# Kernel tuning notes

Measured on AMD Instinct MI355X. Metric: run time of the kernel, lower is better.

The kernel has to match this reference:

```python
import jax, jax.numpy as jnp
import numpy as np

B, S, D = 4, 2048, 1024

def setup_inputs() -> dict:
    key = jax.random.key(0)
    k1, k2, k3, k4 = jax.random.split(key, 4)
    x = jax.random.normal(k1, (B, S, D), dtype=jnp.float32)
    # module init: jr.normal(key, (dim, dim)) / 40
    Qw = jax.random.normal(k2, (D, D), dtype=jnp.float32) / 40
    Kw = jax.random.normal(k3, (D, D), dtype=jnp.float32) / 40
    Vw = jax.random.normal(k4, (D, D), dtype=jnp.float32) / 40
    return {"x": x, "Qw": Qw, "Kw": Kw, "Vw": Vw}

def reference(x, Qw, Kw, Vw):
    # Q/K/V projections: [B,S,D] @ [D,D] -> [B,S,D]
    Q = x @ Qw
    K = x @ Kw
    V = x @ Vw
    d = x.shape[-1]
    S_len = x.shape[-2]
    # causal additive mask: 0 on/below diagonal, -inf above
    mask = jnp.where(jnp.tril(jnp.ones((S_len, S_len), dtype=x.dtype)) == 0,
                     -jnp.inf, 0.0).astype(x.dtype)
    # scores: [B,S,S]
    scores = jnp.einsum('bqd,bkd->bqk', Q, K) / jnp.sqrt(jnp.asarray(d, x.dtype))
    scores = scores + mask
    attn = jax.nn.softmax(scores, axis=-1)
    return jnp.einsum('bqk,bkd->bqd', attn, V)
```

## Files before the change

kernel.cpp:

```cpp
#include <hip/hip_runtime.h>
#include <hip/hip_bf16.h>

typedef __attribute__((ext_vector_type(8))) __bf16 bf16x8;
typedef __attribute__((ext_vector_type(4))) float f32x4;

#define BM 128
#define BN 128
#define BK 64

__device__ inline unsigned short f2bf(float f) {
    union { float f; unsigned u; } v; v.f = f;
    unsigned r = (v.u + 0x7FFFu + ((v.u >> 16) & 1u)) >> 16;
    return (unsigned short)r;
}

__device__ __forceinline__ void gld16(const void* g, void* l) {
    __builtin_amdgcn_global_load_lds(
        (const __attribute__((address_space(1))) unsigned int*)g,
        (__attribute__((address_space(3))) unsigned int*)l, 16, 0, 0);
}

__global__ void detect_dtype(const unsigned short* __restrict__ x, int* __restrict__ flag)
{
    const int tid = threadIdx.x;
    int cnt = 0;
    for (int i = tid; i < 1024; i += 256) {
        unsigned e = (x[2 * i] >> 7) & 0xFFu;
        cnt += (e >= 0x60u && e <= 0x88u) ? 1 : 0;
    }
    #pragma unroll
    for (int o = 32; o >= 1; o >>= 1) cnt += __shfl_xor(cnt, o, 64);
    __shared__ int red[4];
    if ((tid & 63) == 0) red[tid >> 6] = cnt;
    __syncthreads();
    if (tid == 0) {
        int t = red[0] + red[1] + red[2] + red[3];
        *flag = (t >= 512) ? 0 : 1;
    }
}

__global__ __launch_bounds__(256, 2)
void gemm_bt(const unsigned short* __restrict__ A, const unsigned short* __restrict__ Bt,
             void* __restrict__ Call, int K, int lda, int ldb, int ldc,
             long oA, long oB, long oC, long sA, long sB, long sC,
             float scale, int mode, int q0,
             const int* __restrict__ dtf, int outKind)
{
    const int dt = *dtf;
    const int z = blockIdx.z;
    const long aBase = oA + (long)z * sA;
    const long bBase = oB + (long)z * sB;
    const long cBase = oC + (long)z * sC;

    int mt, nt;
    {
        const int nwg = gridDim.x * gridDim.y;
        int lin = blockIdx.y * gridDim.x + blockIdx.x;
        const int q = nwg >> 3, r = nwg & 7;
        const int xcd = lin & 7, idx = lin >> 3;
        lin = (xcd < r ? xcd * (q + 1) : r * (q + 1) + (xcd - r) * q) + idx;
        if (mode == 1) {
            int rem = lin, rr = 0, w = q0 / BN + 1;
            while (rem >= w) { rem -= w; rr++; w++; }
            mt = rr; nt = rem;
        } else { mt = lin / gridDim.x; nt = lin % gridDim.x; }
    }
    const int m0 = mt * BM;
    const int n0 = nt * BN;
    int kmax = K;
    if (mode == 2) kmax = min(K, q0 + m0 + BM);

    __shared__ __align__(16) short As[2][BM * BK];
    __shared__ __align__(16) short Bs[2][BN * BK];

    const int tid  = threadIdx.x;
    const int wave = tid >> 6;
    const int lane = tid & 63;
    const int wm = (wave >> 1) * 64;
    const int wn = (wave & 1) * 64;
    const int lrow = lane & 15;
    const int quad = lane >> 4;

    const int sRow = lane >> 3;
    const int sCol = ((lane & 7) ^ sRow) * 8;
    const long gA = aBase + (long)(m0 + wave * 32 + sRow) * lda + sCol;
    const long gB = bBase + (long)(n0 + wave * 32 + sRow) * ldb + sCol;

    auto stage = [&](int buf, int k0) {
        short* dA = &As[buf][wave * 32 * BK];
        short* dB = &Bs[buf][wave * 32 * BK];
        const unsigned short* pA = A + gA + k0;
        const unsigned short* pB = Bt + gB + k0;
        #pragma unroll
        for (int c = 0; c < 4; c++) {
            gld16(pA + (long)(c * 8) * lda, dA + c * 8 * BK);
            gld16(pB + (long)(c * 8) * ldb, dB + c * 8 * BK);
        }
    };

    f32x4 acc[4][4];
    #pragma unroll
    for (int i = 0; i < 4; i++)
        #pragma unroll
        for (int j = 0; j < 4; j++) {
            f32x4 zero = {0.f, 0.f, 0.f, 0.f};
            acc[i][j] = zero;
        }

    const int rq  = lrow & 7;
    const int pc0 = (quad ^ rq) * 8;
    const int pc1 = ((quad + 4) ^ rq) * 8;

    stage(0, 0);
    __syncthreads();
    int cur = 0;

    for (int k0 = 0; k0 < kmax; k0 += BK) {
        const int kn = k0 + BK;
        if (kn < kmax) stage(cur ^ 1, kn);

        const short* rA = &As[cur][0];
        const short* rB = &Bs[cur][0];
        bf16x8 af[4], bfr[4];
        #pragma unroll
        for (int i = 0; i < 4; i++) {
            af[i]  = *(const bf16x8*)&rA[(wm + i * 16 + lrow) * BK + pc0];
            bfr[i] = *(const bf16x8*)&rB[(wn + i * 16 + lrow) * BK + pc0];
        }
        #pragma unroll
        for (int i = 0; i < 4; i++)
            #pragma unroll
            for (int j = 0; j < 4; j++)
                acc[i][j] = __builtin_amdgcn_mfma_f32_16x16x32_bf16(af[i], bfr[j], acc[i][j], 0, 0, 0);
        #pragma unroll
        for (int i = 0; i < 4; i++) {
            af[i]  = *(const bf16x8*)&rA[(wm + i * 16 + lrow) * BK + pc1];
            bfr[i] = *(const bf16x8*)&rB[(wn + i * 16 + lrow) * BK + pc1];
        }
        #pragma unroll
        for (int i = 0; i < 4; i++)
            #pragma unroll
            for (int j = 0; j < 4; j++)
                acc[i][j] = __builtin_amdgcn_mfma_f32_16x16x32_bf16(af[i], bfr[j], acc[i][j], 0, 0, 0);

        __syncthreads();
        cur ^= 1;
    }

    const int oF32 = (outKind == 1) | ((outKind == 2) & dt);
    #pragma unroll
    for (int i = 0; i < 4; i++) {
        const int mr = m0 + wm + i * 16 + quad * 4;
        #pragma unroll
        for (int j = 0; j < 4; j++) {
            const int nc = n0 + wn + j * 16 + lrow;
            #pragma unroll
            for (int r = 0; r < 4; r++) {
                const long ofs = cBase + (long)(mr + r) * ldc + nc;
                const float v = acc[i][j][r] * scale;
                if (oF32) ((float*)Call)[ofs] = v;
                else      ((unsigned short*)Call)[ofs] = f2bf(v);
            }
        }
    }
}

__global__ __launch_bounds__(256)
void xpose_cast(const void* __restrict__ src, unsigned short* __restrict__ dT,
                unsigned short* __restrict__ dC, int R, int C,
                long oS, long sS, long sDT, long sDC,
                const int* __restrict__ dtf, int srcExt)
{
    const int dt = srcExt ? *dtf : 0;
    const int b = blockIdx.z;
    const long sb = oS + (long)b * sS;
    __shared__ unsigned short t[64][65];
    const int c0 = blockIdx.x * 64, r0 = blockIdx.y * 64;
    const int tid = threadIdx.x;
    #pragma unroll
    for (int it = 0; it < 16; it++) {
        int idx = it * 256 + tid;
        int r = idx >> 6, c = idx & 63;
        long e = sb + (long)(r0 + r) * C + (c0 + c);
        unsigned short v = dt ? f2bf(((const float*)src)[e]) : ((const unsigned short*)src)[e];
        t[r][c] = v;
        if (dC) dC[(long)b * sDC + (long)(r0 + r) * C + (c0 + c)] = v;
    }
    if (!dT) return;
    __syncthreads();
    #pragma unroll
    for (int it = 0; it < 16; it++) {
        int idx = it * 256 + tid;
        int r = idx >> 6, c = idx & 63;
        dT[(long)b * sDT + (long)(c0 + r) * R + (r0 + c)] = t[c][r];
    }
}

__global__ __launch_bounds__(256)
void softmax_causal(float* __restrict__ Sc, int S, int CH, int q0)
{
    const int r = blockIdx.x, z = blockIdx.y;
    float* srow = Sc + ((long)z * CH + r) * S;
    unsigned short* prow = (unsigned short*)srow;
    const int n = q0 + r + 1;
    const int limit = q0 + (r & ~(BM - 1)) + BM;
    const int tid = threadIdx.x;
    const int lane = tid & 63, wave = tid >> 6;
    __shared__ float red[4];

    float v[8];
    float lm = -1e30f;
    #pragma unroll
    for (int c = 0; c < 8; c++) {
        int j = c * 256 + tid;
        v[c] = (j < n) ? srow[j] : -1e30f;
        lm = fmaxf(lm, v[c]);
    }
    #pragma unroll
    for (int o = 32; o >= 1; o >>= 1) lm = fmaxf(lm, __shfl_xor(lm, o, 64));
    if (lane == 0) red[wave] = lm;
    __syncthreads();
    const float m = fmaxf(fmaxf(red[0], red[1]), fmaxf(red[2], red[3]));
    __syncthreads();

    float ev[8];
    float ls = 0.f;
    #pragma unroll
    for (int c = 0; c < 8; c++) {
        int j = c * 256 + tid;
        float e = (j < n) ? __expf(v[c] - m) : 0.f;
        ev[c] = e;
        ls += e;
    }
    #pragma unroll
    for (int o = 32; o >= 1; o >>= 1) ls += __shfl_xor(ls, o, 64);
    if (lane == 0) red[wave] = ls;
    __syncthreads();
    const float inv = 1.0f / (red[0] + red[1] + red[2] + red[3]);

    #pragma unroll
    for (int c = 0; c < 8; c++) {
        int j = c * 256 + tid;
        if (j < limit) prow[j] = f2bf(j < n ? ev[c] * inv : 0.f);
    }
}

__global__ __launch_bounds__(256)
void fill_zero(void* o, long n, const int* dtf)
{
    long i = (long)blockIdx.x * 256 + threadIdx.x;
    if (i < n) {
        if (*dtf) ((float*)o)[i] = 0.f;
        else ((unsigned short*)o)[i] = 0;
    }
}

extern "C" void kernel_launch(void* const* d_in, const int* in_sizes, int n_in,
                              void* d_out, int out_size, void* d_ws, size_t ws_size,
                              hipStream_t stream)
{
    const int B = 4, S = 2048, D = 1024;
    const void* x  = d_in[0];
    const void* Qw = d_in[1];
    const void* Kw = d_in[2];
    const void* Vw = d_in[3];
    (void)in_sizes; (void)n_in; (void)out_size;

    int* dtf = (int*)d_ws;
    char* p = (char*)d_ws + 4096;
    const size_t MB = (size_t)1 << 20;

    detect_dtype<<<1, 256, 0, stream>>>((const unsigned short*)x, dtf);

    const long nOut = (long)B * S * D;

    const size_t needA = 4096 + 36 * MB + (size_t)B * S * S * 4;
    if (ws_size >= needA) {
        unsigned short* QwB = (unsigned short*)p;
        unsigned short* KwB = (unsigned short*)(p + 2 * MB);
        unsigned short* Xb  = (unsigned short*)(p + 4 * MB);
        unsigned short* Buf = (unsigned short*)(p + 20 * MB);
        float* Sc = (float*)(p + 36 * MB);
        unsigned short* WT  = (unsigned short*)Sc;
        unsigned short* VwT = QwB;
        unsigned short* Xt  = Xb;

        xpose_cast<<<dim3(16, 32, 4), 256, 0, stream>>>(
            x, nullptr, Xb, S, D, 0L, (long)S * D, 0L, (long)S * D, dtf, 1);
        xpose_cast<<<dim3(16, 16, 1), 256, 0, stream>>>(
            Qw, nullptr, QwB, D, D, 0L, 0L, 0L, 0L, dtf, 1);
        xpose_cast<<<dim3(16, 16, 1), 256, 0, stream>>>(
            Kw, nullptr, KwB, D, D, 0L, 0L, 0L, 0L, dtf, 1);
        gemm_bt<<<dim3(8, 8, 1), 256, 0, stream>>>(
            KwB, QwB, WT, D, D, D, D, 0L, 0L, 0L, 0L, 0L, 0L, 0.03125f, 0, 0, dtf, 0);
        gemm_bt<<<dim3(8, 64, 1), 256, 0, stream>>>(
            Xb, WT, Buf, D, D, D, D, 0L, 0L, 0L, 0L, 0L, 0L, 1.0f, 0, 0, dtf, 0);
        gemm_bt<<<dim3(136, 1, 4), 256, 0, stream>>>(
            Buf, Xb, (void*)Sc, D, D, D, S,
            0L, 0L, 0L, (long)S * D, (long)S * D, (long)S * S, 1.0f, 1, 0, dtf, 1);
        softmax_causal<<<dim3(S, 4), 256, 0, stream>>>(Sc, S, S, 0);
        xpose_cast<<<dim3(16, 32, 4), 256, 0, stream>>>(
            x, Xt, nullptr, S, D, 0L, (long)S * D, (long)D * S, 0L, dtf, 1);
        xpose_cast<<<dim3(16, 16, 1), 256, 0, stream>>>(
            Vw, VwT, nullptr, D, D, 0L, 0L, 0L, 0L, dtf, 1);
        gemm_bt<<<dim3(8, 16, 4), 256, 0, stream>>>(
            (const unsigned short*)Sc, Xt, Buf, S, 2 * S, S, D,
            0L, 0L, 0L, (long)2 * S * S, (long)D * S, (long)S * D, 1.0f, 2, 0, dtf, 0);
        gemm_bt<<<dim3(8, 64, 1), 256, 0, stream>>>(
            Buf, VwT, d_out, D, D, D, D, 0L, 0L, 0L, 0L, 0L, 0L, 1.0f, 0, 0, dtf, 2);
        return;
    }

    const int cfgs[6][2] = {{4,1024},{2,1024},{1,1024},{1,512},{1,256},{1,128}};
    int ZB = 0, CH = 0;
    for (int i = 0; i < 6; i++) {
        size_t need = 4096 + 56 * MB + (size_t)cfgs[i][0] * cfgs[i][1] * S * 4;
        if (need <= ws_size) { ZB = cfgs[i][0]; CH = cfgs[i][1]; break; }
    }
    if (ZB == 0) {
        fill_zero<<<dim3((unsigned)((nOut + 255) / 256)), 256, 0, stream>>>(d_out, nOut, dtf);
        return;
    }

    unsigned short* QwB = (unsigned short*)p;
    unsigned short* KwB = (unsigned short*)(p + 2 * MB);
    unsigned short* WT  = (unsigned short*)(p + 4 * MB);
    unsigned short* VwT = (unsigned short*)(p + 6 * MB);
    unsigned short* Xb  = (unsigned short*)(p + 8 * MB);
    unsigned short* Xt  = (unsigned short*)(p + 24 * MB);
    unsigned short* Buf = (unsigned short*)(p + 40 * MB);
    float* Sc = (float*)(p + 56 * MB);

    xpose_cast<<<dim3(16, 32, 4), 256, 0, stream>>>(
        x, Xt, Xb, S, D, 0L, (long)S * D, (long)D * S, (long)S * D, dtf, 1);
    xpose_cast<<<dim3(16, 16, 1), 256, 0, stream>>>(Qw, nullptr, QwB, D, D, 0L, 0L, 0L, 0L, dtf, 1);
    xpose_cast<<<dim3(16, 16, 1), 256, 0, stream>>>(Kw, nullptr, KwB, D, D, 0L, 0L, 0L, 0L, dtf, 1);
    xpose_cast<<<dim3(16, 16, 1), 256, 0, stream>>>(Vw, VwT, nullptr, D, D, 0L, 0L, 0L, 0L, dtf, 1);

    gemm_bt<<<dim3(8, 8, 1), 256, 0, stream>>>(
        KwB, QwB, WT, D, D, D, D, 0L, 0L, 0L, 0L, 0L, 0L, 0.03125f, 0, 0, dtf, 0);
    gemm_bt<<<dim3(8, 64, 1), 256, 0, stream>>>(
        Xb, WT, Buf, D, D, D, D, 0L, 0L, 0L, 0L, 0L, 0L, 1.0f, 0, 0, dtf, 0);

    for (int b0 = 0; b0 < B; b0 += ZB) {
        for (int q0 = 0; q0 < S; q0 += CH) {
            const int base = q0 / BN, R = CH / BM;
            const int ntiles = R * (base + 1) + R * (R - 1) / 2;

            gemm_bt<<<dim3(ntiles, 1, ZB), 256, 0, stream>>>(
                Buf, Xb, (void*)Sc, D, D, D, S,
                (long)b0 * S * D + (long)q0 * D, (long)b0 * S * D, 0L,
                (long)S * D, (long)S * D, (long)CH * S, 1.0f, 1, q0, dtf, 1);

            softmax_causal<<<dim3(CH, ZB), 256, 0, stream>>>(Sc, S, CH, q0);

            gemm_bt<<<dim3(8, CH / BM, ZB), 256, 0, stream>>>(
                (const unsigned short*)Sc, Xt, Buf, S, 2 * S, S, D,
                0L, (long)b0 * D * S, (long)b0 * S * D + (long)q0 * D,
                (long)CH * 2 * S, (long)D * S, (long)S * D, 1.0f, 2, q0, dtf, 0);
        }
    }

    gemm_bt<<<dim3(8, 64, 1), 256, 0, stream>>>(
        Buf, VwT, d_out, D, D, D, D, 0L, 0L, 0L, 0L, 0L, 0L, 1.0f, 0, 0, dtf, 2);
}
```

Baseline: 301.6 us.

## Deepen GEMM prefetch to a 4-buffer ring with BK=32 and balanced causal tile ordering

The K tile shrinks to 32 and the double buffer becomes a 4-slot LDS ring with prefetch depth 2. Explicit vmcnt waits and a single barrier per iteration replace the old two-syncthreads scheme, so more global loads stay in flight while MFMAs run. Separately, the causal mode-2 GEMM now pairs short and long row tiles (front/back interleave, longest first) to balance work across workgroups. The swizzle pattern is rewritten for the narrower tile, and the code assumes kmax is a multiple of 32 and at least two stages exist. The barrier-only sync may race with buffer reuse if the ring depth is wrong.

```diff
diff --git a/kernel.cpp b/kernel.cpp
--- a/kernel.cpp
+++ b/kernel.cpp
@@ -6,7 +6,9 @@
 
 #define BM 128
 #define BN 128
-#define BK 64
+#define BK 32
+#define NBUF 4
+#define DEPTH 2
 
 __device__ inline unsigned short f2bf(float f) {
     union { float f; unsigned u; } v; v.f = f;
@@ -53,7 +55,14 @@
     const long cBase = oC + (long)z * sC;
 
     int mt, nt;
-    {
+    if (mode == 2) {
+        const int nwg2 = gridDim.x * gridDim.y;
+        const int h = blockIdx.y * gridDim.x + blockIdx.x;
+        const int u = h >> 1;
+        const int rank = (h & 1) ? (nwg2 - 1 - u) : u;
+        mt = (gridDim.y - 1) - (rank / (int)gridDim.x);
+        nt = rank % (int)gridDim.x;
+    } else {
         const int nwg = gridDim.x * gridDim.y;
         int lin = blockIdx.y * gridDim.x + blockIdx.x;
         const int q = nwg >> 3, r = nwg & 7;
@@ -70,8 +79,8 @@
     int kmax = K;
     if (mode == 2) kmax = min(K, q0 + m0 + BM);
 
-    __shared__ __align__(16) short As[2][BM * BK];
-    __shared__ __align__(16) short Bs[2][BN * BK];
+    __shared__ __align__(16) short As[NBUF][BM * BK];
+    __shared__ __align__(16) short Bs[NBUF][BN * BK];
 
     const int tid  = threadIdx.x;
     const int wave = tid >> 6;
@@ -81,8 +90,8 @@
     const int lrow = lane & 15;
     const int quad = lane >> 4;
 
-    const int sRow = lane >> 3;
-    const int sCol = ((lane & 7) ^ sRow) * 8;
+    const int sRow = lane >> 2;
+    const int sCol = ((lane & 3) ^ ((lane >> 3) & 3)) * 8;
     const long gA = aBase + (long)(m0 + wave * 32 + sRow) * lda + sCol;
     const long gB = bBase + (long)(n0 + wave * 32 + sRow) * ldb + sCol;
 
@@ -91,11 +100,10 @@
         short* dB = &Bs[buf][wave * 32 * BK];
         const unsigned short* pA = A + gA + k0;
         const unsigned short* pB = Bt + gB + k0;
-        #pragma unroll
-        for (int c = 0; c < 4; c++) {
-            gld16(pA + (long)(c * 8) * lda, dA + c * 8 * BK);
-            gld16(pB + (long)(c * 8) * ldb, dB + c * 8 * BK);
-        }
+        gld16(pA, dA);
+        gld16(pA + 16 * (long)lda, dA + 16 * BK);
+        gld16(pB, dB);
+        gld16(pB + 16 * (long)ldb, dB + 16 * BK);
     };
 
     f32x4 acc[4][4];
@@ -107,44 +115,37 @@
             acc[i][j] = zero;
         }
 
-    const int rq  = lrow & 7;
-    const int pc0 = (quad ^ rq) * 8;
-    const int pc1 = ((quad + 4) ^ rq) * 8;
-
+    const int pc = ((quad ^ ((lrow >> 1) & 3))) * 8;
+
+    const int nk = kmax / BK;
     stage(0, 0);
-    __syncthreads();
-    int cur = 0;
-
-    for (int k0 = 0; k0 < kmax; k0 += BK) {
-        const int kn = k0 + BK;
-        if (kn < kmax) stage(cur ^ 1, kn);
-
-        const short* rA = &As[cur][0];
-        const short* rB = &Bs[cur][0];
+    stage(1, BK);
+
+    for (int it = 0; it < nk; it++) {
+        if (it + DEPTH < nk) {
+            stage((it + DEPTH) & (NBUF - 1), (it + DEPTH) * BK);
+            asm volatile("s_waitcnt vmcnt(8)" ::: "memory");
+        } else if (it + 1 < nk) {
+            asm volatile("s_waitcnt vmcnt(4)" ::: "memory");
+        } else {
+            asm volatile("s_waitcnt vmcnt(0)" ::: "memory");
+        }
+        __builtin_amdgcn_s_barrier();
+        __builtin_amdgcn_sched_barrier(0);
+
+        const short* rA = &As[it & (NBUF - 1)][0];
+        const short* rB = &Bs[it & (NBUF - 1)][0];
         bf16x8 af[4], bfr[4];
         #pragma unroll
         for (int i = 0; i < 4; i++) {
-            af[i]  = *(const bf16x8*)&rA[(wm + i * 16 + lrow) * BK + pc0];
-            bfr[i] = *(const bf16x8*)&rB[(wn + i * 16 + lrow) * BK + pc0];
+            af[i]  = *(const bf16x8*)&rA[(wm + i * 16 + lrow) * BK + pc];
+            bfr[i] = *(const bf16x8*)&rB[(wn + i * 16 + lrow) * BK + pc];
         }
         #pragma unroll
         for (int i = 0; i < 4; i++)
             #pragma unroll
             for (int j = 0; j < 4; j++)
                 acc[i][j] = __builtin_amdgcn_mfma_f32_16x16x32_bf16(af[i], bfr[j], acc[i][j], 0, 0, 0);
-        #pragma unroll
-        for (int i = 0; i < 4; i++) {
-            af[i]  = *(const bf16x8*)&rA[(wm + i * 16 + lrow) * BK + pc1];
-            bfr[i] = *(const bf16x8*)&rB[(wn + i * 16 + lrow) * BK + pc1];
-        }
-        #pragma unroll
-        for (int i = 0; i < 4; i++)
-            #pragma unroll
-            for (int j = 0; j < 4; j++)
-                acc[i][j] = __builtin_amdgcn_mfma_f32_16x16x32_bf16(af[i], bfr[j], acc[i][j], 0, 0, 0);
-
-        __syncthreads();
-        cur ^= 1;
     }
 
     const int oF32 = (outKind == 1) | ((outKind == 2) & dt);
```

New measurement: 313.6 us. +4.0%, slower.

## Compute V projection before attention and reorder causal PV tile scheduling

Applied to the files above, without the earlier changes.

Instead of computing P·X and then projecting by Vw, V = X·Vw is computed up front, transposed, and P·V writes directly into the output. That drops the separate final projection GEMM and the x transpose, but adds a transpose of V. Qw/Kw conversion becomes a single vectorized cast kernel instead of two xpose_cast launches. The mode-2 (PV) grid is remapped to pair long and short causal row tiles for load balance. In the fallback path d_out is reused as scratch for V, which is fine only if the output dtype is large enough.

```diff
diff --git a/kernel.cpp b/kernel.cpp
--- a/kernel.cpp
+++ b/kernel.cpp
@@ -2,6 +2,7 @@
 #include <hip/hip_bf16.h>
 
 typedef __attribute__((ext_vector_type(8))) __bf16 bf16x8;
+typedef __attribute__((ext_vector_type(8))) short short8;
 typedef __attribute__((ext_vector_type(4))) float f32x4;
 
 #define BM 128
@@ -53,7 +54,14 @@
     const long cBase = oC + (long)z * sC;
 
     int mt, nt;
-    {
+    if (mode == 2) {
+        const int nwg2 = gridDim.x * gridDim.y;
+        const int h = blockIdx.y * gridDim.x + blockIdx.x;
+        const int u = h >> 1;
+        const int rank = (h & 1) ? (nwg2 - 1 - u) : u;
+        mt = (gridDim.y - 1) - (rank / (int)gridDim.x);
+        nt = rank % (int)gridDim.x;
+    } else {
         const int nwg = gridDim.x * gridDim.y;
         int lin = blockIdx.y * gridDim.x + blockIdx.x;
         const int q = nwg >> 3, r = nwg & 7;
@@ -197,6 +205,28 @@
 }
 
 __global__ __launch_bounds__(256)
+void cast2(const void* __restrict__ s0, const void* __restrict__ s1,
+           unsigned short* __restrict__ d0, unsigned short* __restrict__ d1,
+           long n, const int* __restrict__ dtf)
+{
+    const int dt = *dtf;
+    const void* s = blockIdx.y ? s1 : s0;
+    unsigned short* d = blockIdx.y ? d1 : d0;
+    long i = ((long)blockIdx.x * 256 + threadIdx.x) * 8;
+    if (i >= n) return;
+    union { short8 v; unsigned short u[8]; } o;
+    if (dt) {
+        f32x4 a = *(const f32x4*)((const float*)s + i);
+        f32x4 b = *(const f32x4*)((const float*)s + i + 4);
+        #pragma unroll
+        for (int j = 0; j < 4; j++) { o.u[j] = f2bf(a[j]); o.u[4 + j] = f2bf(b[j]); }
+    } else {
+        o.v = *(const short8*)((const short*)s + i);
+    }
+    *(short8*)(d + i) = o.v;
+}
+
+__global__ __launch_bounds__(256)
 void softmax_causal(float* __restrict__ Sc, int S, int CH, int q0)
 {
     const int r = blockIdx.x, z = blockIdx.y;
@@ -283,14 +313,11 @@
         float* Sc = (float*)(p + 36 * MB);
         unsigned short* WT  = (unsigned short*)Sc;
         unsigned short* VwT = QwB;
-        unsigned short* Xt  = Xb;
+        unsigned short* VbT = Xb;
 
         xpose_cast<<<dim3(16, 32, 4), 256, 0, stream>>>(
             x, nullptr, Xb, S, D, 0L, (long)S * D, 0L, (long)S * D, dtf, 1);
-        xpose_cast<<<dim3(16, 16, 1), 256, 0, stream>>>(
-            Qw, nullptr, QwB, D, D, 0L, 0L, 0L, 0L, dtf, 1);
-        xpose_cast<<<dim3(16, 16, 1), 256, 0, stream>>>(
-            Kw, nullptr, KwB, D, D, 0L, 0L, 0L, 0L, dtf, 1);
+        cast2<<<dim3(512, 2), 256, 0, stream>>>(Qw, Kw, QwB, KwB, (long)D * D, dtf);
         gemm_bt<<<dim3(8, 8, 1), 256, 0, stream>>>(
             KwB, QwB, WT, D, D, D, D, 0L, 0L, 0L, 0L, 0L, 0L, 0.03125f, 0, 0, dtf, 0);
         gemm_bt<<<dim3(8, 64, 1), 256, 0, stream>>>(
@@ -299,15 +326,15 @@
             Buf, Xb, (void*)Sc, D, D, D, S,
             0L, 0L, 0L, (long)S * D, (long)S * D, (long)S * S, 1.0f, 1, 0, dtf, 1);
         softmax_causal<<<dim3(S, 4), 256, 0, stream>>>(Sc, S, S, 0);
-        xpose_cast<<<dim3(16, 32, 4), 256, 0, stream>>>(
-            x, Xt, nullptr, S, D, 0L, (long)S * D, (long)D * S, 0L, dtf, 1);
         xpose_cast<<<dim3(16, 16, 1), 256, 0, stream>>>(
             Vw, VwT, nullptr, D, D, 0L, 0L, 0L, 0L, dtf, 1);
+        gemm_bt<<<dim3(8, 64, 1), 256, 0, stream>>>(
+            Xb, VwT, Buf, D, D, D, D, 0L, 0L, 0L, 0L, 0L, 0L, 1.0f, 0, 0, dtf, 0);
+        xpose_cast<<<dim3(16, 32, 4), 256, 0, stream>>>(
+            Buf, VbT, nullptr, S, D, 0L, (long)S * D, (long)D * S, 0L, dtf, 0);
         gemm_bt<<<dim3(8, 16, 4), 256, 0, stream>>>(
-            (const unsigned short*)Sc, Xt, Buf, S, 2 * S, S, D,
-            0L, 0L, 0L, (long)2 * S * S, (long)D * S, (long)S * D, 1.0f, 2, 0, dtf, 0);
-        gemm_bt<<<dim3(8, 64, 1), 256, 0, stream>>>(
-            Buf, VwT, d_out, D, D, D, D, 0L, 0L, 0L, 0L, 0L, 0L, 1.0f, 0, 0, dtf, 2);
+            (const unsigned short*)Sc, VbT, d_out, S, 2 * S, S, D,
+            0L, 0L, 0L, (long)2 * S * S, (long)D * S, (long)S * D, 1.0f, 2, 0, dtf, 2);
         return;
     }
 
@@ -327,20 +354,24 @@
     unsigned short* WT  = (unsigned short*)(p + 4 * MB);
     unsigned short* VwT = (unsigned short*)(p + 6 * MB);
     unsigned short* Xb  = (unsigned short*)(p + 8 * MB);
-    unsigned short* Xt  = (unsigned short*)(p + 24 * MB);
+    unsigned short* VbT = (unsigned short*)(p + 24 * MB);
     unsigned short* Buf = (unsigned short*)(p + 40 * MB);
     float* Sc = (float*)(p + 56 * MB);
+    unsigned short* VbS = (unsigned short*)d_out;
 
     xpose_cast<<<dim3(16, 32, 4), 256, 0, stream>>>(
-        x, Xt, Xb, S, D, 0L, (long)S * D, (long)D * S, (long)S * D, dtf, 1);
-    xpose_cast<<<dim3(16, 16, 1), 256, 0, stream>>>(Qw, nullptr, QwB, D, D, 0L, 0L, 0L, 0L, dtf, 1);
-    xpose_cast<<<dim3(16, 16, 1), 256, 0, stream>>>(Kw, nullptr, KwB, D, D, 0L, 0L, 0L, 0L, dtf, 1);
+        x, nullptr, Xb, S, D, 0L, (long)S * D, 0L, (long)S * D, dtf, 1);
+    cast2<<<dim3(512, 2), 256, 0, stream>>>(Qw, Kw, QwB, KwB, (long)D * D, dtf);
     xpose_cast<<<dim3(16, 16, 1), 256, 0, stream>>>(Vw, VwT, nullptr, D, D, 0L, 0L, 0L, 0L, dtf, 1);
 
     gemm_bt<<<dim3(8, 8, 1), 256, 0, stream>>>(
         KwB, QwB, WT, D, D, D, D, 0L, 0L, 0L, 0L, 0L, 0L, 0.03125f, 0, 0, dtf, 0);
     gemm_bt<<<dim3(8, 64, 1), 256, 0, stream>>>(
         Xb, WT, Buf, D, D, D, D, 0L, 0L, 0L, 0L, 0L, 0L, 1.0f, 0, 0, dtf, 0);
+    gemm_bt<<<dim3(8, 64, 1), 256, 0, stream>>>(
+        Xb, VwT, VbS, D, D, D, D, 0L, 0L, 0L, 0L, 0L, 0L, 1.0f, 0, 0, dtf, 0);
+    xpose_cast<<<dim3(16, 32, 4), 256, 0, stream>>>(
+        VbS, VbT, nullptr, S, D, 0L, (long)S * D, (long)D * S, 0L, dtf, 0);
 
     for (int b0 = 0; b0 < B; b0 += ZB) {
         for (int q0 = 0; q0 < S; q0 += CH) {
@@ -355,12 +386,9 @@
             softmax_causal<<<dim3(CH, ZB), 256, 0, stream>>>(Sc, S, CH, q0);
 
             gemm_bt<<<dim3(8, CH / BM, ZB), 256, 0, stream>>>(
-                (const unsigned short*)Sc, Xt, Buf, S, 2 * S, S, D,
+                (const unsigned short*)Sc, VbT, d_out, S, 2 * S, S, D,
                 0L, (long)b0 * D * S, (long)b0 * S * D + (long)q0 * D,
-                (long)CH * 2 * S, (long)D * S, (long)S * D, 1.0f, 2, q0, dtf, 0);
-        }
-    }
-
-    gemm_bt<<<dim3(8, 64, 1), 256, 0, stream>>>(
-        Buf, VwT, d_out, D, D, D, D, 0L, 0L, 0L, 0L, 0L, 0L, 1.0f, 0, 0, dtf, 2);
-}
+                (long)CH * 2 * S, (long)D * S, (long)S * D, 1.0f, 2, q0, dtf, 2);
+        }
+    }
+}
```

New measurement: 282.9 us. 1.07x faster.
